# Kernel optimization log

Measured on AMD Instinct MI355X. Metric: run time of the kernel, lower is better.

Reference implementation:

```python
import jax, jax.numpy as jnp
import numpy as np

VOCAB = 50257
EMBED_DIM = 768
NUM_TUNE = 1024


def setup_inputs() -> dict:
    key = jax.random.key(0)
    k_ids, k_tune, k_base, k_train = jax.random.split(key, 4)
    input_ids = jax.random.randint(k_ids, (8, 4096), 0, VOCAB, dtype=jnp.int64)
    tune_ids = jnp.sort(jax.random.randint(k_tune, (NUM_TUNE,), 0, VOCAB, dtype=jnp.int64))
    base_weight = jax.random.normal(k_base, (VOCAB, EMBED_DIM), dtype=jnp.float32)
    # In the torch module train_weight is initialized from base rows; independent init is fine for a numeric baseline.
    train_weight = jax.random.normal(k_train, (NUM_TUNE, EMBED_DIM), dtype=jnp.float32)
    return {"input_ids": input_ids, "tune_ids": tune_ids,
            "base_weight": base_weight, "train_weight": train_weight}


def reference(input_ids, tune_ids, base_weight, train_weight):
    # Precompute id -> train-row mapping (replaces the torch.isin + python-loop dict lookup).
    id2row = jnp.full((VOCAB,), -1, dtype=jnp.int32)
    id2row = id2row.at[tune_ids].set(jnp.arange(NUM_TUNE, dtype=jnp.int32))
    out = base_weight[input_ids]                      # [B, S, D] gather
    rows = id2row[input_ids]                          # [B, S] train-row index or -1
    mask = rows >= 0
    override = train_weight[jnp.maximum(rows, 0)]     # [B, S, D]
    return jnp.where(mask[..., None], override, out)
```

## Files before the change

### kernel.cpp

```cpp
#include <hip/hip_runtime.h>


#define EMBED_DIM   768
#define WAVES_PER_BLOCK 4
#define TOK_PER_WAVE 4
#define TOK_PER_BLOCK (WAVES_PER_BLOCK * TOK_PER_WAVE)
#define MISS_FLAG 0x40000000

typedef __attribute__((ext_vector_type(4))) float f4;

__global__ __launch_bounds__(256) void build_rows_kernel(
    const int* __restrict__ input_ids, const int* __restrict__ tune_ids,
    int* __restrict__ enc, int num_tokens, int num_tune)
{
    __shared__ int lds_tune[2048];
    const bool use_lds = (num_tune <= 2048);
    if (use_lds) {
        for (int i = threadIdx.x; i < num_tune; i += 256)
            lds_tune[i] = tune_ids[i];
        __syncthreads();
    }
    const int t = blockIdx.x * 256 + threadIdx.x;
    if (t >= num_tokens) return;

    const int tok = input_ids[t];
    const int* tab = use_lds ? lds_tune : tune_ids;
    int lo = 0, hi = num_tune;
    while (lo < hi) {
        const int mid = (lo + hi) >> 1;
        if (tab[mid] <= tok) lo = mid + 1;
        else                 hi = mid;
    }
    const int cand = lo - 1;
    const bool hit = (cand >= 0) && (tab[cand] == tok);
    enc[t] = hit ? cand : (MISS_FLAG | tok);
}

__device__ __forceinline__ const f4* decode(int e, const float* base, const float* train) {
    return (e & MISS_FLAG)
        ? (const f4*)(base  + (size_t)(e & (MISS_FLAG - 1)) * EMBED_DIM)
        : (const f4*)(train + (size_t)e * EMBED_DIM);
}

__global__ __launch_bounds__(256) void copy_rows_kernel(
    const int* __restrict__ enc,
    const float* __restrict__ base_weight, const float* __restrict__ train_weight,
    float* __restrict__ out, int num_tokens)
{
    const int wave = threadIdx.x >> 6;
    const int lane = threadIdx.x & 63;
    const int tb   = (blockIdx.x * WAVES_PER_BLOCK + wave) * TOK_PER_WAVE;
    if (tb >= num_tokens) return;

    if (tb + TOK_PER_WAVE <= num_tokens) {
        const int4 e4 = *(const int4*)(enc + tb);
        const f4* s0 = decode(e4.x, base_weight, train_weight);
        const f4* s1 = decode(e4.y, base_weight, train_weight);
        const f4* s2 = decode(e4.z, base_weight, train_weight);
        const f4* s3 = decode(e4.w, base_weight, train_weight);

        f4 v[12];
        #pragma unroll
        for (int c = 0; c < 3; ++c) v[0 * 3 + c] = s0[lane + c * 64];
        #pragma unroll
        for (int c = 0; c < 3; ++c) v[1 * 3 + c] = s1[lane + c * 64];
        #pragma unroll
        for (int c = 0; c < 3; ++c) v[2 * 3 + c] = s2[lane + c * 64];
        #pragma unroll
        for (int c = 0; c < 3; ++c) v[3 * 3 + c] = s3[lane + c * 64];

        #pragma unroll
        for (int t = 0; t < 4; ++t) {
            f4* dst = (f4*)(out + (size_t)(tb + t) * EMBED_DIM);
            #pragma unroll
            for (int c = 0; c < 3; ++c)
                __builtin_nontemporal_store(v[t * 3 + c], dst + lane + c * 64);
        }
    } else {
        for (int t = tb; t < num_tokens; ++t) {
            const f4* src = decode(enc[t], base_weight, train_weight);
            f4* dst = (f4*)(out + (size_t)t * EMBED_DIM);
            #pragma unroll
            for (int c = 0; c < 3; ++c)
                __builtin_nontemporal_store(src[lane + c * 64], dst + lane + c * 64);
        }
    }
}

extern "C" void kernel_launch(void* const* d_in, const int* in_sizes, int n_in,
                              void* d_out, int out_size, void* d_ws, size_t ws_size,
                              hipStream_t stream) {
    const int*   input_ids    = (const int*)d_in[0];
    const int*   tune_ids     = (const int*)d_in[1];
    const float* base_weight  = (const float*)d_in[2];
    const float* train_weight = (const float*)d_in[3];
    float*       out          = (float*)d_out;
    int*         enc          = (int*)d_ws;

    const int num_tokens = in_sizes[0];
    const int num_tune   = in_sizes[1];

    const int gridA = (num_tokens + 255) / 256;
    build_rows_kernel<<<gridA, 256, 0, stream>>>(input_ids, tune_ids, enc,
                                                 num_tokens, num_tune);

    const int gridB = (num_tokens + TOK_PER_BLOCK - 1) / TOK_PER_BLOCK;
    copy_rows_kernel<<<gridB, 256, 0, stream>>>(enc, base_weight, train_weight,
                                                out, num_tokens);
}
```

Measured before the change: 245.9 us.

## Fuse tune-id binary search into the row-copy kernel

Merges the lookup kernel and the copy kernel into a single launch. Each wave binary-searches its four tokens directly against tune_ids staged in LDS, then uses shuffles to hand the encoded row to every lane. This drops a kernel launch and the round trip of the encoded index buffer through global memory. In exchange, every 16-token block now reloads the whole tune table into LDS (2048 blocks each loading 4KB) and pays a barrier before it can issue its gathers.

```diff
diff --git a/kernel.cpp b/kernel.cpp
--- a/kernel.cpp
+++ b/kernel.cpp
@@ -1,40 +1,14 @@
 #include <hip/hip_runtime.h>
 
 
-#define EMBED_DIM   768
+#define EMBED_DIM 768
 #define WAVES_PER_BLOCK 4
 #define TOK_PER_WAVE 4
 #define TOK_PER_BLOCK (WAVES_PER_BLOCK * TOK_PER_WAVE)
 #define MISS_FLAG 0x40000000
+#define MAX_TUNE_LDS 1024
 
 typedef __attribute__((ext_vector_type(4))) float f4;
-
-__global__ __launch_bounds__(256) void build_rows_kernel(
-    const int* __restrict__ input_ids, const int* __restrict__ tune_ids,
-    int* __restrict__ enc, int num_tokens, int num_tune)
-{
-    __shared__ int lds_tune[2048];
-    const bool use_lds = (num_tune <= 2048);
-    if (use_lds) {
-        for (int i = threadIdx.x; i < num_tune; i += 256)
-            lds_tune[i] = tune_ids[i];
-        __syncthreads();
-    }
-    const int t = blockIdx.x * 256 + threadIdx.x;
-    if (t >= num_tokens) return;
-
-    const int tok = input_ids[t];
-    const int* tab = use_lds ? lds_tune : tune_ids;
-    int lo = 0, hi = num_tune;
-    while (lo < hi) {
-        const int mid = (lo + hi) >> 1;
-        if (tab[mid] <= tok) lo = mid + 1;
-        else                 hi = mid;
-    }
-    const int cand = lo - 1;
-    const bool hit = (cand >= 0) && (tab[cand] == tok);
-    enc[t] = hit ? cand : (MISS_FLAG | tok);
-}
 
 __device__ __forceinline__ const f4* decode(int e, const float* base, const float* train) {
     return (e & MISS_FLAG)
@@ -42,22 +16,50 @@
         : (const f4*)(train + (size_t)e * EMBED_DIM);
 }
 
-__global__ __launch_bounds__(256) void copy_rows_kernel(
-    const int* __restrict__ enc,
-    const float* __restrict__ base_weight, const float* __restrict__ train_weight,
-    float* __restrict__ out, int num_tokens)
+__global__ __launch_bounds__(256) void split_embedding_fused(
+    const int* __restrict__ input_ids,
+    const int* __restrict__ tune_ids,
+    const float* __restrict__ base_weight,
+    const float* __restrict__ train_weight,
+    float* __restrict__ out,
+    int num_tokens, int num_tune)
 {
+    __shared__ int lds_tune[MAX_TUNE_LDS];
+    const bool use_lds = (num_tune <= MAX_TUNE_LDS);
+    if (use_lds) {
+        for (int i = threadIdx.x; i < num_tune; i += 256)
+            lds_tune[i] = tune_ids[i];
+    }
+    __syncthreads();
+
     const int wave = threadIdx.x >> 6;
     const int lane = threadIdx.x & 63;
     const int tb   = (blockIdx.x * WAVES_PER_BLOCK + wave) * TOK_PER_WAVE;
     if (tb >= num_tokens) return;
 
+    const int* __restrict__ tab = use_lds ? lds_tune : tune_ids;
+
     if (tb + TOK_PER_WAVE <= num_tokens) {
-        const int4 e4 = *(const int4*)(enc + tb);
-        const f4* s0 = decode(e4.x, base_weight, train_weight);
-        const f4* s1 = decode(e4.y, base_weight, train_weight);
-        const f4* s2 = decode(e4.z, base_weight, train_weight);
-        const f4* s3 = decode(e4.w, base_weight, train_weight);
+        const int4 t4 = *(const int4*)(input_ids + tb);
+
+        const int my = (lane & 3) == 0 ? t4.x : (lane & 3) == 1 ? t4.y
+                     : (lane & 3) == 2 ? t4.z : t4.w;
+        int lo = 0, hi = num_tune;
+        while (lo < hi) {
+            const int mid = (lo + hi) >> 1;
+            if (tab[mid] <= my) lo = mid + 1;
+            else                hi = mid;
+        }
+        const int cand = lo - 1;
+        const bool hit = (cand >= 0) && (tab[cand] == my);
+        const int enc  = hit ? cand : (MISS_FLAG | my);
+
+        const int e0 = __shfl(enc, 0), e1 = __shfl(enc, 1);
+        const int e2 = __shfl(enc, 2), e3 = __shfl(enc, 3);
+        const f4* s0 = decode(e0, base_weight, train_weight);
+        const f4* s1 = decode(e1, base_weight, train_weight);
+        const f4* s2 = decode(e2, base_weight, train_weight);
+        const f4* s3 = decode(e3, base_weight, train_weight);
 
         f4 v[12];
         #pragma unroll
@@ -78,7 +80,18 @@
         }
     } else {
         for (int t = tb; t < num_tokens; ++t) {
-            const f4* src = decode(enc[t], base_weight, train_weight);
+            const int tok = input_ids[t];
+            int lo = 0, hi = num_tune;
+            while (lo < hi) {
+                const int mid = (lo + hi) >> 1;
+                if (tab[mid] <= tok) lo = mid + 1;
+                else                 hi = mid;
+            }
+            const int cand = lo - 1;
+            const bool hit = (cand >= 0) && (tab[cand] == tok);
+            const f4* src = hit
+                ? (const f4*)(train_weight + (size_t)cand * EMBED_DIM)
+                : (const f4*)(base_weight  + (size_t)tok  * EMBED_DIM);
             f4* dst = (f4*)(out + (size_t)t * EMBED_DIM);
             #pragma unroll
             for (int c = 0; c < 3; ++c)
@@ -95,16 +108,11 @@
     const float* base_weight  = (const float*)d_in[2];
     const float* train_weight = (const float*)d_in[3];
     float*       out          = (float*)d_out;
-    int*         enc          = (int*)d_ws;
 
     const int num_tokens = in_sizes[0];
     const int num_tune   = in_sizes[1];
 
-    const int gridA = (num_tokens + 255) / 256;
-    build_rows_kernel<<<gridA, 256, 0, stream>>>(input_ids, tune_ids, enc,
-                                                 num_tokens, num_tune);
-
-    const int gridB = (num_tokens + TOK_PER_BLOCK - 1) / TOK_PER_BLOCK;
-    copy_rows_kernel<<<gridB, 256, 0, stream>>>(enc, base_weight, train_weight,
-                                                out, num_tokens);
+    const int grid = (num_tokens + TOK_PER_BLOCK - 1) / TOK_PER_BLOCK;
+    split_embedding_fused<<<grid, 256, 0, stream>>>(
+        input_ids, tune_ids, base_weight, train_weight, out, num_tokens, num_tune);
 }
```

New measurement: 245.1 us. About the same (-0.3%).
